# Kernel optimization log

Hardware: AMD Instinct MI355X
Metric: run time of the kernel (lower is better)

## Reference

```python
import jax, jax.numpy as jnp
import numpy as np

V, E, H, A, L = 32000, 512, 1024, 1024, 2
B, T, S = 16, 64, 64


def gru_cell(x, h, W_ih, W_hh, b_ih, b_hh):
    # torch GRUCell math: gates ordered (r, z, n)
    gx = x @ W_ih.T + b_ih
    gh = h @ W_hh.T + b_hh
    xr, xz, xn = jnp.split(gx, 3, axis=-1)
    hr, hz, hn = jnp.split(gh, 3, axis=-1)
    r = jax.nn.sigmoid(xr + hr)
    z = jax.nn.sigmoid(xz + hz)
    n = jnp.tanh(xn + r * hn)
    return (1.0 - z) * n + z * h


def setup_inputs() -> dict:
    key = jax.random.key(0)
    ks = jax.random.split(key, 20)
    s = 0.02
    return {
        "tgt": jax.random.randint(ks[0], (B, T), 0, V),
        "hidden": jax.random.normal(ks[1], (L, B, H), jnp.float32) * 0.1,
        "encoder_outputs": jax.random.normal(ks[2], (B, S, H), jnp.float32),
        "emb": jax.random.normal(ks[3], (V, E), jnp.float32) * s,
        "Wq": jax.random.normal(ks[4], (H, A), jnp.float32) * s,
        "Wk": jax.random.normal(ks[5], (H, A), jnp.float32) * s,
        "v_att": jax.random.normal(ks[6], (A,), jnp.float32) * s,
        "W_ih0": jax.random.normal(ks[7], (3 * H, E + H), jnp.float32) * s,
        "W_hh0": jax.random.normal(ks[8], (3 * H, H), jnp.float32) * s,
        "b_ih0": jnp.zeros((3 * H,), jnp.float32),
        "b_hh0": jnp.zeros((3 * H,), jnp.float32),
        "W_ih1": jax.random.normal(ks[9], (3 * H, H), jnp.float32) * s,
        "W_hh1": jax.random.normal(ks[10], (3 * H, H), jnp.float32) * s,
        "b_ih1": jnp.zeros((3 * H,), jnp.float32),
        "b_hh1": jnp.zeros((3 * H,), jnp.float32),
        "W_out": jax.random.normal(ks[11], (V, H), jnp.float32) * s,
        "b_out": jnp.zeros((V,), jnp.float32),
    }


def reference(tgt, hidden, encoder_outputs, emb, Wq, Wk, v_att,
              W_ih0, W_hh0, b_ih0, b_hh0, W_ih1, W_hh1, b_ih1, b_hh1,
              W_out, b_out):
    # Teacher forcing (ratio=1.0), dropout in eval mode (identity).
    keys_proj = jnp.einsum('bsh,ha->bsa', encoder_outputs, Wk)  # precompute W_k K
    emb_tok = emb[tgt]  # [B,T,E]

    def step(carry, x_t):
        h0, h1 = carry  # each [B,H]
        # Bahdanau attention: query = last-layer hidden
        q = jnp.einsum('bh,ha->ba', h1, Wq)
        scores = jnp.einsum('bsa,a->bs', jnp.tanh(q[:, None, :] + keys_proj), v_att)
        attn = jax.nn.softmax(scores, axis=-1)
        ctx = jnp.einsum('bs,bsh->bh', attn, encoder_outputs)
        rnn_in = jnp.concatenate([x_t, ctx], axis=-1)  # [B, E+H]
        h0n = gru_cell(rnn_in, h0, W_ih0, W_hh0, b_ih0, b_hh0)
        h1n = gru_cell(h0n, h1, W_ih1, W_hh1, b_ih1, b_hh1)
        logits = h1n @ W_out.T + b_out  # [B,V]
        return (h0n, h1n), logits

    (_, _), logits = jax.lax.scan(step, (hidden[0], hidden[1]),
                                  jnp.swapaxes(emb_tok, 0, 1))  # xs: [T,B,E]
    return jnp.swapaxes(logits, 0, 1)  # [B,T,V]
```

## Files before the change

kernel.cpp:

```cpp
#include <hip/hip_runtime.h>
#include <hip/hip_bf16.h>
#include <math.h>

typedef __bf16 bf16x8 __attribute__((ext_vector_type(8)));
typedef float  f32x4  __attribute__((ext_vector_type(4)));

#define MFMA16 __builtin_amdgcn_mfma_f32_16x16x32_bf16

__device__ __forceinline__ float sigm(float x){ return 1.0f/(1.0f+expf(-x)); }
__device__ __forceinline__ f32x4 ld4(const float* p){ return *(const f32x4*)p; }
__device__ __forceinline__ void split2(float x, __bf16* h, __bf16* l){
  __bf16 hh = (__bf16)x; *h = hh; *l = (__bf16)(x - (float)hh);
}

__global__ __launch_bounds__(256) void k_transpose(const float* __restrict__ in,
                                                   float* __restrict__ out, int R, int C){
  __shared__ float tile[32][33];
  int c0 = blockIdx.x*32, r0 = blockIdx.y*32;
  int tx = threadIdx.x & 31, ty = threadIdx.x >> 5;
  for(int i=ty;i<32;i+=8) tile[i][tx] = in[(size_t)(r0+i)*C + c0+tx];
  __syncthreads();
  for(int i=ty;i<32;i+=8) out[(size_t)(c0+i)*R + r0+tx] = tile[tx][i];
}

__global__ __launch_bounds__(256) void k_gather(const int* __restrict__ tgt,
                                                const float* __restrict__ emb,
                                                float* __restrict__ emb_tok){
  int m = blockIdx.x;
  int t = m >> 4, b = m & 15;
  int row = tgt[b*64 + t];
  const float* src = emb + (size_t)row*512;
  float* dst = emb_tok + (size_t)m*512;
  for(int e=threadIdx.x;e<512;e+=256) dst[e] = src[e];
}

__global__ __launch_bounds__(256) void k_gemm_s(
    const float* __restrict__ A, int lda,
    const float* __restrict__ Bt, int ldb,
    const float* __restrict__ bias,
    float* __restrict__ C, int N, int K)
{
  __shared__ __align__(16) __bf16 Ash[128][40];
  __shared__ __align__(16) __bf16 Asl[128][40];
  __shared__ __align__(16) __bf16 Bsh[64][40];
  __shared__ __align__(16) __bf16 Bsl[64][40];
  int tid = threadIdx.x;
  int m0 = blockIdx.x*128, n0 = blockIdx.y*64;
  int lane = tid & 63, wave = tid >> 6;
  int wr = wave >> 1, wc = wave & 1;
  int qq = lane >> 4, rr = lane & 15;
  f32x4 acc[4][2] = {};
  int ar = tid >> 1, ak = (tid & 1)*16;
  int br = tid >> 2, bk = (tid & 3)*8;
  for(int k0=0;k0<K;k0+=32){
    const float* ap = A + (size_t)(m0+ar)*lda + k0 + ak;
    f32x4 a0 = ld4(ap), a1 = ld4(ap+4), a2 = ld4(ap+8), a3 = ld4(ap+12);
    const float* bp = Bt + (size_t)(n0+br)*ldb + k0 + bk;
    f32x4 b0 = ld4(bp), b1 = ld4(bp+4);
    __syncthreads();
    #pragma unroll
    for(int e=0;e<4;++e){
      split2(a0[e], &Ash[ar][ak+e],    &Asl[ar][ak+e]);
      split2(a1[e], &Ash[ar][ak+4+e],  &Asl[ar][ak+4+e]);
      split2(a2[e], &Ash[ar][ak+8+e],  &Asl[ar][ak+8+e]);
      split2(a3[e], &Ash[ar][ak+12+e], &Asl[ar][ak+12+e]);
      split2(b0[e], &Bsh[br][bk+e],    &Bsl[br][bk+e]);
      split2(b1[e], &Bsh[br][bk+4+e],  &Bsl[br][bk+4+e]);
    }
    __syncthreads();
    bf16x8 afh[4], afl[4], bfh[2], bfl[2];
    #pragma unroll
    for(int mi=0;mi<4;++mi){
      afh[mi] = *(const bf16x8*)&Ash[wr*64 + mi*16 + rr][qq*8];
      afl[mi] = *(const bf16x8*)&Asl[wr*64 + mi*16 + rr][qq*8];
    }
    #pragma unroll
    for(int ni=0;ni<2;++ni){
      bfh[ni] = *(const bf16x8*)&Bsh[wc*32 + ni*16 + rr][qq*8];
      bfl[ni] = *(const bf16x8*)&Bsl[wc*32 + ni*16 + rr][qq*8];
    }
    #pragma unroll
    for(int mi=0;mi<4;++mi)
      #pragma unroll
      for(int ni=0;ni<2;++ni){
        acc[mi][ni] = MFMA16(afh[mi], bfh[ni], acc[mi][ni], 0,0,0);
        acc[mi][ni] = MFMA16(afl[mi], bfh[ni], acc[mi][ni], 0,0,0);
        acc[mi][ni] = MFMA16(afh[mi], bfl[ni], acc[mi][ni], 0,0,0);
      }
  }
  #pragma unroll
  for(int mi=0;mi<4;++mi)
    #pragma unroll
    for(int ni=0;ni<2;++ni)
      #pragma unroll
      for(int i=0;i<4;++i){
        int m = m0 + wr*64 + mi*16 + qq*4 + i;
        int n = n0 + wc*32 + ni*16 + rr;
        C[(size_t)m*N + n] = acc[mi][ni][i] + (bias? bias[n] : 0.f);
      }
}

__global__ __launch_bounds__(256) void k_pack_w(const float* __restrict__ W,
                                                __bf16* __restrict__ Wp){
  int jt = blockIdx.x, tid = threadIdx.x;
  #pragma unroll
  for(int it=0; it<8; ++it){
    int pos = it*256 + tid;
    int kt = pos>>6, l = pos&63;
    const float* src = W + (size_t)(jt*16 + (l&15))*1024 + kt*32 + (l>>4)*8;
    f32x4 s0 = ld4(src), s1 = ld4(src+4);
    bf16x8 vh, vl;
    #pragma unroll
    for(int e=0;e<4;++e){
      __bf16 h, lo;
      split2(s0[e], &h, &lo); vh[e]   = h; vl[e]   = lo;
      split2(s1[e], &h, &lo); vh[4+e] = h; vl[4+e] = lo;
    }
    __bf16* dst = Wp + ((size_t)(jt*32 + kt))*1024 + l*8;
    *(bf16x8*)dst       = vh;
    *(bf16x8*)(dst+512) = vl;
  }
}

__global__ __launch_bounds__(256) void k_pack_wT(const float* __restrict__ W, int ldw,
                                                 __bf16* __restrict__ Wp){
  int jt = blockIdx.x, tid = threadIdx.x;
  #pragma unroll
  for(int it=0; it<8; ++it){
    int pos = it*256 + tid;
    int kt = pos>>6, l = pos&63;
    int j = jt*16 + (l&15);
    int kbase = kt*32 + (l>>4)*8;
    bf16x8 vh, vl;
    #pragma unroll
    for(int e=0;e<8;++e){
      float x = W[(size_t)(kbase+e)*ldw + j];
      __bf16 h = (__bf16)x;
      vh[e] = h; vl[e] = (__bf16)(x - (float)h);
    }
    __bf16* dst = Wp + ((size_t)(jt*32 + kt))*1024 + l*8;
    *(bf16x8*)dst       = vh;
    *(bf16x8*)(dst+512) = vl;
  }
}

__global__ __launch_bounds__(256) void k_split_h(const float* __restrict__ hidden,
    __bf16* __restrict__ h0h, __bf16* __restrict__ h0l,
    __bf16* __restrict__ h1h, __bf16* __restrict__ h1l){
  int i = blockIdx.x*256 + threadIdx.x;
  float x = hidden[i];
  if(i < 16384) split2(x, &h0h[i], &h0l[i]);
  else { int j = i - 16384; split2(x, &h1h[j], &h1l[j]); }
}

__global__ __launch_bounds__(256) void k_cvt16(const float* __restrict__ in,
                                               __bf16* __restrict__ out){
  int i = blockIdx.x*256 + threadIdx.x;
  const float* p = in + (size_t)i*8;
  f32x4 f0 = ld4(p), f1 = ld4(p+4);
  bf16x8 v;
  #pragma unroll
  for(int e=0;e<4;++e){ v[e] = (__bf16)f0[e]; v[4+e] = (__bf16)f1[e]; }
  *(bf16x8*)(out + (size_t)i*8) = v;
}

__device__ __forceinline__ void gemv_w8(const __bf16* __restrict__ hh,
                                        const __bf16* __restrict__ hl,
                                        const __bf16* __restrict__ Wp, int jt,
                                        float* __restrict__ out, int ldo,
                                        f32x4* red){
  int tid = threadIdx.x, lane = tid & 63, w = tid >> 6;
  const __bf16* Ah = hh + (lane&15)*1024 + (lane>>4)*8;
  const __bf16* Al = hl + (lane&15)*1024 + (lane>>4)*8;
  const __bf16* Bp = Wp + ((size_t)jt*32 + w*4)*1024 + lane*8;
  f32x4 acc = {0.f,0.f,0.f,0.f};
  #pragma unroll
  for(int kk=0;kk<4;++kk){
    int k0 = (w*4 + kk)*32;
    bf16x8 ah = *(const bf16x8*)(Ah + k0);
    bf16x8 al = *(const bf16x8*)(Al + k0);
    bf16x8 bh = *(const bf16x8*)(Bp + kk*1024);
    bf16x8 bl = *(const bf16x8*)(Bp + kk*1024 + 512);
    acc = MFMA16(ah, bh, acc, 0,0,0);
    acc = MFMA16(al, bh, acc, 0,0,0);
    acc = MFMA16(ah, bl, acc, 0,0,0);
  }
  red[w*64 + lane] = acc;
  __syncthreads();
  if(tid < 64){
    f32x4 s = red[tid];
    #pragma unroll
    for(int k=1;k<8;++k) s += red[k*64 + tid];
    int j = jt*16 + (tid & 15);
    #pragma unroll
    for(int i=0;i<4;++i) out[(size_t)((tid>>4)*4 + i)*ldo + j] = s[i];
  }
}

__global__ __launch_bounds__(512) void k_boot(const __bf16* __restrict__ hh,
                                              const __bf16* __restrict__ hl,
                                              const __bf16* __restrict__ Wp,
                                              float* __restrict__ gh0){
  __shared__ f32x4 red[512];
  gemv_w8(hh, hl, Wp, blockIdx.x, gh0, 3072, red);
}

__global__ __launch_bounds__(512) void k_SA(
    const __bf16* __restrict__ h1h, const __bf16* __restrict__ h1l,
    const __bf16* __restrict__ Whh1p, const __bf16* __restrict__ Wqp,
    const float* __restrict__ kp, const float* __restrict__ v_att,
    float* __restrict__ gh1, float* __restrict__ parts)
{
  __shared__ f32x4 red[512];
  __shared__ float qs[16][16];
  int blk = blockIdx.x, tid = threadIdx.x;
  if(blk < 192){ gemv_w8(h1h, h1l, Whh1p, blk, gh1, 3072, red); return; }
  int slice = blk - 192;
  {
    int lane = tid & 63, w = tid >> 6;
    const __bf16* Ah = h1h + (lane&15)*1024 + (lane>>4)*8;
    const __bf16* Al = h1l + (lane&15)*1024 + (lane>>4)*8;
    const __bf16* Bp = Wqp + ((size_t)slice*32 + w*4)*1024 + lane*8;
    f32x4 acc = {0.f,0.f,0.f,0.f};
    #pragma unroll
    for(int kk=0;kk<4;++kk){
      int k0 = (w*4 + kk)*32;
      bf16x8 ah = *(const bf16x8*)(Ah + k0);
      bf16x8 al = *(const bf16x8*)(Al + k0);
      bf16x8 bh = *(const bf16x8*)(Bp + kk*1024);
      bf16x8 bl = *(const bf16x8*)(Bp + kk*1024 + 512);
      acc = MFMA16(ah, bh, acc, 0,0,0);
      acc = MFMA16(al, bh, acc, 0,0,0);
      acc = MFMA16(ah, bl, acc, 0,0,0);
    }
    red[w*64 + lane] = acc;
    __syncthreads();
    if(tid < 64){
      f32x4 s = red[tid];
      #pragma unroll
      for(int k=1;k<8;++k) s += red[k*64 + tid];
      #pragma unroll
      for(int i=0;i<4;++i) qs[(tid>>4)*4 + i][tid&15] = s[i];
    }
    __syncthreads();
  }
  const float* vp = v_att + slice*16;
  f32x4 v0 = ld4(vp), v1 = ld4(vp+4), v2 = ld4(vp+8), v3 = ld4(vp+12);
  #pragma unroll
  for(int r=0;r<2;++r){
    int pair = r*512 + tid;
    int b = pair >> 6;
    const float* kpr = kp + (size_t)pair*1024 + slice*16;
    f32x4 c0 = ld4(kpr), c1 = ld4(kpr+4), c2 = ld4(kpr+8), c3 = ld4(kpr+12);
    float acc = 0.f;
    #pragma unroll
    for(int e=0;e<4;++e){
      acc += v0[e]*tanhf(qs[b][e]     + c0[e]);
      acc += v1[e]*tanhf(qs[b][4+e]   + c1[e]);
      acc += v2[e]*tanhf(qs[b][8+e]   + c2[e]);
      acc += v3[e]*tanhf(qs[b][12+e]  + c3[e]);
    }
    parts[(size_t)slice*1024 + pair] = acc;
  }
}

__global__ __launch_bounds__(512) void k_SB(int t,
    const float* __restrict__ parts, const float* __restrict__ EW,
    const float* __restrict__ GX0x, const float* __restrict__ gh0,
    const float* __restrict__ b_hh0,
    const float* __restrict__ h0_in, float* __restrict__ h0_out,
    __bf16* __restrict__ h0h, __bf16* __restrict__ h0l)
{
  __shared__ float ssum[256][2];
  __shared__ float sc[4][64];
  __shared__ float sden[4];
  __shared__ float part[8][4][16][3];
  int blk = blockIdx.x, tid = threadIdx.x;
  int jt = blk >> 2, bq = blk & 3;
  {
    int p = tid >> 1, hf = tid & 1;
    int pair = bq*256 + p;
    const float* pp = parts + (size_t)(hf*32)*1024 + pair;
    float s = 0.f;
    #pragma unroll
    for(int k=0;k<32;++k) s += pp[(size_t)k*1024];
    ssum[p][hf] = s;
  }
  __syncthreads();
  if(tid < 256) sc[tid>>6][tid&63] = expf(ssum[tid][0] + ssum[tid][1]);
  __syncthreads();
  if(tid < 4){
    float d = 0.f;
    #pragma unroll
    for(int s2=0;s2<64;++s2) d += sc[tid][s2];
    sden[tid] = d;
  }
  __syncthreads();
  int lane = tid & 63, w = tid >> 6;
  int bl = lane >> 4, jl = lane & 15;
  int b = bq*4 + bl, col = jt*16 + jl;
  float a0=0.f, a1=0.f, a2=0.f;
  const float* ewp = EW + ((size_t)(b*64 + w*8))*3072 + col;
  #pragma unroll
  for(int si=0; si<8; ++si){
    float e = sc[bl][w*8 + si];
    const float* r2 = ewp + (size_t)si*3072;
    a0 += e*r2[0]; a1 += e*r2[1024]; a2 += e*r2[2048];
  }
  part[w][bl][jl][0]=a0; part[w][bl][jl][1]=a1; part[w][bl][jl][2]=a2;
  __syncthreads();
  if(tid < 64){
    int bl2 = tid >> 4, jl2 = tid & 15;
    int b2 = bq*4 + bl2, j = jt*16 + jl2;
    float xr=0.f, xz=0.f, xn=0.f;
    #pragma unroll
    for(int k=0;k<8;++k){ xr+=part[k][bl2][jl2][0]; xz+=part[k][bl2][jl2][1]; xn+=part[k][bl2][jl2][2]; }
    float inv = 1.0f / sden[bl2];
    const float* gx = GX0x + ((size_t)t*16 + b2)*3072 + j;
    const float* g0 = gh0 + (size_t)b2*3072 + j;
    float r = sigm(xr*inv + gx[0]    + g0[0]    + b_hh0[j]);
    float z = sigm(xz*inv + gx[1024] + g0[1024] + b_hh0[1024+j]);
    float n = tanhf(xn*inv + gx[2048] + r*(g0[2048] + b_hh0[2048+j]));
    float hnew = (1.f-z)*n + z*h0_in[b2*1024 + j];
    h0_out[b2*1024 + j] = hnew;
    split2(hnew, &h0h[b2*1024 + j], &h0l[b2*1024 + j]);
  }
}

__global__ __launch_bounds__(512) void k_SC(int t,
    const __bf16* __restrict__ h0h, const __bf16* __restrict__ h0l,
    const __bf16* __restrict__ Wih1p, const __bf16* __restrict__ Whh0p,
    const float* __restrict__ b_ih1, const float* __restrict__ b_hh1,
    const float* __restrict__ gh1,
    const float* __restrict__ h1_in, float* __restrict__ h1_out,
    __bf16* __restrict__ h1h, __bf16* __restrict__ h1l,
    __bf16* __restrict__ Hb, float* __restrict__ gh0)
{
  __shared__ f32x4 red[1536];
  __shared__ float xg[3][16][16];
  int blk = blockIdx.x, tid = threadIdx.x;
  if(blk >= 64){ gemv_w8(h0h, h0l, Whh0p, blk-64, gh0, 3072, red); return; }
  int lane = tid & 63, w = tid >> 6;
  const __bf16* Ah = h0h + (lane&15)*1024 + (lane>>4)*8;
  const __bf16* Al = h0l + (lane&15)*1024 + (lane>>4)*8;
  #pragma unroll
  for(int g=0; g<3; ++g){
    const __bf16* Bp = Wih1p + ((size_t)(g*64 + blk)*32 + w*4)*1024 + lane*8;
    f32x4 acc = {0.f,0.f,0.f,0.f};
    #pragma unroll
    for(int kk=0;kk<4;++kk){
      int k0 = (w*4 + kk)*32;
      bf16x8 ah = *(const bf16x8*)(Ah + k0);
      bf16x8 al = *(const bf16x8*)(Al + k0);
      bf16x8 bh = *(const bf16x8*)(Bp + kk*1024);
      bf16x8 bl = *(const bf16x8*)(Bp + kk*1024 + 512);
      acc = MFMA16(ah, bh, acc, 0,0,0);
      acc = MFMA16(al, bh, acc, 0,0,0);
      acc = MFMA16(ah, bl, acc, 0,0,0);
    }
    red[g*512 + w*64 + lane] = acc;
  }
  __syncthreads();
  if(tid < 192){
    int g = tid >> 6, tt = tid & 63;
    f32x4 s = red[g*512 + tt];
    #pragma unroll
    for(int k=1;k<8;++k) s += red[g*512 + k*64 + tt];
    #pragma unroll
    for(int i=0;i<4;++i) xg[g][(tt>>4)*4 + i][tt&15] = s[i];
  }
  __syncthreads();
  if(tid < 256){
    int b = tid >> 4, jl = tid & 15, j = blk*16 + jl;
    float xr = xg[0][b][jl] + b_ih1[j];
    float xz = xg[1][b][jl] + b_ih1[1024+j];
    float xn = xg[2][b][jl] + b_ih1[2048+j];
    const float* g1 = gh1 + (size_t)b*3072 + j;
    float r = sigm(xr + g1[0]    + b_hh1[j]);
    float z = sigm(xz + g1[1024] + b_hh1[1024+j]);
    float n = tanhf(xn + r*(g1[2048] + b_hh1[2048+j]));
    float hnew = (1.f-z)*n + z*h1_in[b*1024 + j];
    h1_out[b*1024 + j] = hnew;
    split2(hnew, &h1h[b*1024 + j], &h1l[b*1024 + j]);
    Hb[((size_t)t*16 + b)*1024 + j] = (__bf16)hnew;
  }
}

__global__ __launch_bounds__(512) void k_logits(
    const __bf16* __restrict__ Hb, const __bf16* __restrict__ Wb,
    const float* __restrict__ b_out, float* __restrict__ out)
{
  int c = blockIdx.x & 7, j = blockIdx.x >> 3;
  int x = j & 3, y = (j >> 2)*8 + c;
  if(y >= 250) return;
  int tm0 = x*256, tn0 = y*128;
  __shared__ __align__(16) __bf16 As[256][40];
  __shared__ __align__(16) __bf16 Bs[128][40];
  int tid = threadIdx.x;
  int lane = tid & 63, wave = tid >> 6;
  int wr = wave >> 1, wc = wave & 1;
  int qq = lane >> 4, rr = lane & 15;
  f32x4 acc[4][4] = {};
  int ar = tid >> 2, ak = (tid & 3) * 8;
  for(int k0=0;k0<1024;k0+=32){
    bf16x8 a0v = *(const bf16x8*)(Hb + (size_t)(tm0+ar)*1024     + k0 + ak);
    bf16x8 a1v = *(const bf16x8*)(Hb + (size_t)(tm0+ar+128)*1024 + k0 + ak);
    bf16x8 bv  = *(const bf16x8*)(Wb + (size_t)(tn0+ar)*1024     + k0 + ak);
    __syncthreads();
    *(bf16x8*)&As[ar][ak]     = a0v;
    *(bf16x8*)&As[ar+128][ak] = a1v;
    *(bf16x8*)&Bs[ar][ak]     = bv;
    __syncthreads();
    bf16x8 af[4], bfr[4];
    #pragma unroll
    for(int mi=0;mi<4;++mi) af[mi]  = *(const bf16x8*)&As[wr*64 + mi*16 + rr][qq*8];
    #pragma unroll
    for(int ni=0;ni<4;++ni) bfr[ni] = *(const bf16x8*)&Bs[wc*64 + ni*16 + rr][qq*8];
    #pragma unroll
    for(int mi=0;mi<4;++mi)
      #pragma unroll
      for(int ni=0;ni<4;++ni)
        acc[mi][ni] = MFMA16(af[mi], bfr[ni], acc[mi][ni], 0,0,0);
  }
  #pragma unroll
  for(int mi=0;mi<4;++mi)
    #pragma unroll
    for(int ni=0;ni<4;++ni)
      #pragma unroll
      for(int i=0;i<4;++i){
        int m = tm0 + wr*64 + mi*16 + qq*4 + i;
        int v = tn0 + wc*64 + ni*16 + rr;
        int bb = m & 15, tt = m >> 4;
        out[((size_t)bb*64 + tt)*32000 + v] = acc[mi][ni][i] + b_out[v];
      }
}

extern "C" void kernel_launch(void* const* d_in, const int* in_sizes, int n_in,
                              void* d_out, int out_size, void* d_ws, size_t ws_size,
                              hipStream_t stream){
  const int*   tgt    = (const int*)d_in[0];
  const float* hidden = (const float*)d_in[1];
  const float* enc    = (const float*)d_in[2];
  const float* emb    = (const float*)d_in[3];
  const float* Wq     = (const float*)d_in[4];
  const float* Wk     = (const float*)d_in[5];
  const float* v_att  = (const float*)d_in[6];
  const float* W_ih0  = (const float*)d_in[7];
  const float* W_hh0  = (const float*)d_in[8];
  const float* b_ih0  = (const float*)d_in[9];
  const float* b_hh0  = (const float*)d_in[10];
  const float* W_ih1  = (const float*)d_in[11];
  const float* W_hh1  = (const float*)d_in[12];
  const float* b_ih1  = (const float*)d_in[13];
  const float* b_hh1  = (const float*)d_in[14];
  const float* W_out  = (const float*)d_in[15];
  const float* b_out  = (const float*)d_in[16];
  float* out = (float*)d_out;

  float* ws = (float*)d_ws;
  size_t off = 0;
  auto alloc = [&](size_t n){ float* p = ws + off; off += n; return p; };
  float*  kp     = alloc((size_t)1024*1024);
  float*  GX0x   = alloc((size_t)1024*3072);
  float*  EW     = alloc((size_t)1024*3072);
  __bf16* Whh0p  = (__bf16*)alloc((size_t)3072*1024);
  __bf16* Whh1p  = (__bf16*)alloc((size_t)3072*1024);
  __bf16* Wih1p  = (__bf16*)alloc((size_t)3072*1024);
  __bf16* Wqp    = (__bf16*)alloc((size_t)1024*1024);
  float*  gh0    = alloc((size_t)16*3072);
  float*  gh1    = alloc((size_t)16*3072);
  float*  parts  = alloc((size_t)64*1024);
  float*  h0A    = alloc((size_t)16*1024);
  float*  h0B    = alloc((size_t)16*1024);
  float*  h1A    = alloc((size_t)16*1024);
  float*  h1B    = alloc((size_t)16*1024);
  __bf16* h0sh   = (__bf16*)alloc((size_t)8192);
  __bf16* h0sl   = (__bf16*)alloc((size_t)8192);
  __bf16* h1sh   = (__bf16*)alloc((size_t)8192);
  __bf16* h1sl   = (__bf16*)alloc((size_t)8192);
  float*  Hb_f   = alloc((size_t)512*1024);
  __bf16* Hb     = (__bf16*)Hb_f;
  float*  emb_tok = Hb_f;
  float*  WT      = EW;
  __bf16* Woutb   = (__bf16*)ws;
  (void)ws_size; (void)in_sizes; (void)n_in; (void)out_size;

  k_gather<<<1024,256,0,stream>>>(tgt, emb, emb_tok);
  k_transpose<<<dim3(32,32),256,0,stream>>>(Wk, WT, 1024, 1024);
  k_gemm_s<<<dim3(8,16),256,0,stream>>>(enc,1024, WT,1024, nullptr, kp, 1024, 1024);
  k_gemm_s<<<dim3(8,48),256,0,stream>>>(emb_tok,512, W_ih0,1536, b_ih0, GX0x, 3072, 512);
  k_gemm_s<<<dim3(8,48),256,0,stream>>>(enc,1024, W_ih0+512,1536, nullptr, EW, 3072, 1024);
  k_pack_wT<<<64,256,0,stream>>>(Wq, 1024, Wqp);
  k_pack_w<<<192,256,0,stream>>>(W_hh0, Whh0p);
  k_pack_w<<<192,256,0,stream>>>(W_hh1, Whh1p);
  k_pack_w<<<192,256,0,stream>>>(W_ih1, Wih1p);
  k_split_h<<<128,256,0,stream>>>(hidden, h0sh, h0sl, h1sh, h1sl);
  k_boot<<<192,512,0,stream>>>(h0sh, h0sl, Whh0p, gh0);

  for(int t=0;t<64;++t){
    const float* h0i = (t==0)? hidden            : ((t&1)? h0A : h0B);
    float*       h0o = (t&1)? h0B : h0A;
    const float* h1i = (t==0)? hidden + 16*1024  : ((t&1)? h1A : h1B);
    float*       h1o = (t&1)? h1B : h1A;
    k_SA<<<256,512,0,stream>>>(h1sh, h1sl, Whh1p, Wqp, kp, v_att, gh1, parts);
    k_SB<<<256,512,0,stream>>>(t, parts, EW, GX0x, gh0, b_hh0, h0i, h0o, h0sh, h0sl);
    k_SC<<<256,512,0,stream>>>(t, h0sh, h0sl, Wih1p, Whh0p, b_ih1, b_hh1, gh1,
                               h1i, h1o, h1sh, h1sl, Hb, gh0);
  }

  k_cvt16<<<16000,256,0,stream>>>(W_out, Woutb);
  k_logits<<<1024,512,0,stream>>>(Hb, Woutb, b_out, out);
}
```

Before: 2.166 ms.

## Stage recurrent GEMV weights via direct global-to-LDS loads and double-buffer logits A tile

```diff
diff --git a/kernel.cpp b/kernel.cpp
--- a/kernel.cpp
+++ b/kernel.cpp
@@ -6,6 +6,8 @@
 typedef float  f32x4  __attribute__((ext_vector_type(4)));
 
 #define MFMA16 __builtin_amdgcn_mfma_f32_16x16x32_bf16
+#define WAIT_VM0()   { asm volatile("s_waitcnt vmcnt(0)" ::: "memory");   __builtin_amdgcn_sched_barrier(0); }
+#define WAIT_LGKM0() { asm volatile("s_waitcnt lgkmcnt(0)" ::: "memory"); __builtin_amdgcn_sched_barrier(0); }
 
 __device__ __forceinline__ float sigm(float x){ return 1.0f/(1.0f+expf(-x)); }
 __device__ __forceinline__ f32x4 ld4(const float* p){ return *(const f32x4*)p; }
@@ -164,33 +166,48 @@
   *(bf16x8*)(out + (size_t)i*8) = v;
 }
 
-__device__ __forceinline__ void gemv_w8(const __bf16* __restrict__ hh,
-                                        const __bf16* __restrict__ hl,
-                                        const __bf16* __restrict__ Wp, int jt,
-                                        float* __restrict__ out, int ldo,
-                                        f32x4* red){
+__device__ __forceinline__ void stage_tile(const __bf16* __restrict__ Wp, int jt,
+                                           char* stage, int w, int lane){
+  const char* gsrc = (const char*)Wp + (size_t)jt*65536 + (size_t)w*8192 + lane*16;
+  char* ldst = stage + w*8192;
+  #pragma unroll
+  for(int i=0;i<8;++i)
+    __builtin_amdgcn_global_load_lds(
+      (const __attribute__((address_space(1))) unsigned int*)(gsrc + i*1024),
+      (__attribute__((address_space(3))) unsigned int*)(ldst + i*1024), 16, 0, 0);
+}
+
+__device__ __forceinline__ void gemv_lds(const __bf16* __restrict__ hh,
+                                         const __bf16* __restrict__ hl,
+                                         const __bf16* __restrict__ Wp, int jt,
+                                         char* stage, float* __restrict__ out, int ldo){
   int tid = threadIdx.x, lane = tid & 63, w = tid >> 6;
   const __bf16* Ah = hh + (lane&15)*1024 + (lane>>4)*8;
   const __bf16* Al = hl + (lane&15)*1024 + (lane>>4)*8;
-  const __bf16* Bp = Wp + ((size_t)jt*32 + w*4)*1024 + lane*8;
+  bf16x8 ah[4], al[4];
+  #pragma unroll
+  for(int kk=0;kk<4;++kk){
+    int k0 = (w*4+kk)*32;
+    ah[kk] = *(const bf16x8*)(Ah + k0);
+    al[kk] = *(const bf16x8*)(Al + k0);
+  }
+  stage_tile(Wp, jt, stage, w, lane);
+  WAIT_VM0();
   f32x4 acc = {0.f,0.f,0.f,0.f};
   #pragma unroll
   for(int kk=0;kk<4;++kk){
-    int k0 = (w*4 + kk)*32;
-    bf16x8 ah = *(const bf16x8*)(Ah + k0);
-    bf16x8 al = *(const bf16x8*)(Al + k0);
-    bf16x8 bh = *(const bf16x8*)(Bp + kk*1024);
-    bf16x8 bl = *(const bf16x8*)(Bp + kk*1024 + 512);
-    acc = MFMA16(ah, bh, acc, 0,0,0);
-    acc = MFMA16(al, bh, acc, 0,0,0);
-    acc = MFMA16(ah, bl, acc, 0,0,0);
-  }
-  red[w*64 + lane] = acc;
+    bf16x8 bh = *(const bf16x8*)(stage + w*8192 + kk*2048 + lane*16);
+    bf16x8 bl = *(const bf16x8*)(stage + w*8192 + kk*2048 + 1024 + lane*16);
+    acc = MFMA16(ah[kk], bh, acc, 0,0,0);
+    acc = MFMA16(al[kk], bh, acc, 0,0,0);
+    acc = MFMA16(ah[kk], bl, acc, 0,0,0);
+  }
+  *(f32x4*)(stage + w*8192 + lane*16) = acc;
   __syncthreads();
   if(tid < 64){
-    f32x4 s = red[tid];
-    #pragma unroll
-    for(int k=1;k<8;++k) s += red[k*64 + tid];
+    f32x4 s = *(const f32x4*)(stage + tid*16);
+    #pragma unroll
+    for(int k=1;k<8;++k) s += *(const f32x4*)(stage + k*8192 + tid*16);
     int j = jt*16 + (tid & 15);
     #pragma unroll
     for(int i=0;i<4;++i) out[(size_t)((tid>>4)*4 + i)*ldo + j] = s[i];
@@ -201,8 +218,8 @@
                                               const __bf16* __restrict__ hl,
                                               const __bf16* __restrict__ Wp,
                                               float* __restrict__ gh0){
-  __shared__ f32x4 red[512];
-  gemv_w8(hh, hl, Wp, blockIdx.x, gh0, 3072, red);
+  __shared__ __align__(16) char stage[65536];
+  gemv_lds(hh, hl, Wp, blockIdx.x, stage, gh0, 3072);
 }
 
 __global__ __launch_bounds__(512) void k_SA(
@@ -211,39 +228,45 @@
     const float* __restrict__ kp, const float* __restrict__ v_att,
     float* __restrict__ gh1, float* __restrict__ parts)
 {
-  __shared__ f32x4 red[512];
-  __shared__ float qs[16][16];
+  __shared__ __align__(16) char stage[65536];
   int blk = blockIdx.x, tid = threadIdx.x;
-  if(blk < 192){ gemv_w8(h1h, h1l, Whh1p, blk, gh1, 3072, red); return; }
+  if(blk < 192){ gemv_lds(h1h, h1l, Whh1p, blk, stage, gh1, 3072); return; }
   int slice = blk - 192;
+  int lane = tid & 63, w = tid >> 6;
   {
-    int lane = tid & 63, w = tid >> 6;
     const __bf16* Ah = h1h + (lane&15)*1024 + (lane>>4)*8;
     const __bf16* Al = h1l + (lane&15)*1024 + (lane>>4)*8;
-    const __bf16* Bp = Wqp + ((size_t)slice*32 + w*4)*1024 + lane*8;
+    bf16x8 ah[4], al[4];
+    #pragma unroll
+    for(int kk=0;kk<4;++kk){
+      int k0 = (w*4+kk)*32;
+      ah[kk] = *(const bf16x8*)(Ah + k0);
+      al[kk] = *(const bf16x8*)(Al + k0);
+    }
+    stage_tile(Wqp, slice, stage, w, lane);
+    WAIT_VM0();
     f32x4 acc = {0.f,0.f,0.f,0.f};
     #pragma unroll
     for(int kk=0;kk<4;++kk){
-      int k0 = (w*4 + kk)*32;
-      bf16x8 ah = *(const bf16x8*)(Ah + k0);
-      bf16x8 al = *(const bf16x8*)(Al + k0);
-      bf16x8 bh = *(const bf16x8*)(Bp + kk*1024);
-      bf16x8 bl = *(const bf16x8*)(Bp + kk*1024 + 512);
-      acc = MFMA16(ah, bh, acc, 0,0,0);
-      acc = MFMA16(al, bh, acc, 0,0,0);
-      acc = MFMA16(ah, bl, acc, 0,0,0);
-    }
-    red[w*64 + lane] = acc;
+      bf16x8 bh = *(const bf16x8*)(stage + w*8192 + kk*2048 + lane*16);
+      bf16x8 bl = *(const bf16x8*)(stage + w*8192 + kk*2048 + 1024 + lane*16);
+      acc = MFMA16(ah[kk], bh, acc, 0,0,0);
+      acc = MFMA16(al[kk], bh, acc, 0,0,0);
+      acc = MFMA16(ah[kk], bl, acc, 0,0,0);
+    }
+    *(f32x4*)(stage + w*8192 + lane*16) = acc;
     __syncthreads();
     if(tid < 64){
-      f32x4 s = red[tid];
+      f32x4 s = *(const f32x4*)(stage + tid*16);
       #pragma unroll
-      for(int k=1;k<8;++k) s += red[k*64 + tid];
+      for(int k=1;k<8;++k) s += *(const f32x4*)(stage + k*8192 + tid*16);
+      float* qsp = (float*)(stage + 1024);
       #pragma unroll
-      for(int i=0;i<4;++i) qs[(tid>>4)*4 + i][tid&15] = s[i];
+      for(int i=0;i<4;++i) qsp[((tid>>4)*4 + i)*16 + (tid&15)] = s[i];
     }
     __syncthreads();
   }
+  const float* qsp = (const float*)(stage + 1024);
   const float* vp = v_att + slice*16;
   f32x4 v0 = ld4(vp), v1 = ld4(vp+4), v2 = ld4(vp+8), v3 = ld4(vp+12);
   #pragma unroll
@@ -252,13 +275,14 @@
     int b = pair >> 6;
     const float* kpr = kp + (size_t)pair*1024 + slice*16;
     f32x4 c0 = ld4(kpr), c1 = ld4(kpr+4), c2 = ld4(kpr+8), c3 = ld4(kpr+12);
+    const float* qb = qsp + b*16;
     float acc = 0.f;
     #pragma unroll
     for(int e=0;e<4;++e){
-      acc += v0[e]*tanhf(qs[b][e]     + c0[e]);
-      acc += v1[e]*tanhf(qs[b][4+e]   + c1[e]);
-      acc += v2[e]*tanhf(qs[b][8+e]   + c2[e]);
-      acc += v3[e]*tanhf(qs[b][12+e]  + c3[e]);
+      acc += v0[e]*tanhf(qb[e]     + c0[e]);
+      acc += v1[e]*tanhf(qb[4+e]   + c1[e]);
+      acc += v2[e]*tanhf(qb[8+e]   + c2[e]);
+      acc += v3[e]*tanhf(qb[12+e]  + c3[e]);
     }
     parts[(size_t)slice*1024 + pair] = acc;
   }
@@ -278,7 +302,7 @@
   int blk = blockIdx.x, tid = threadIdx.x;
   int jt = blk >> 2, bq = blk & 3;
   {
-    int p = tid >> 1, hf = tid & 1;
+    int hf = tid >> 8, p = tid & 255;
     int pair = bq*256 + p;
     const float* pp = parts + (size_t)(hf*32)*1024 + pair;
     float s = 0.f;
@@ -336,45 +360,62 @@
     __bf16* __restrict__ h1h, __bf16* __restrict__ h1l,
     __bf16* __restrict__ Hb, float* __restrict__ gh0)
 {
-  __shared__ f32x4 red[1536];
-  __shared__ float xg[3][16][16];
+  __shared__ __align__(16) char stage[65536];
   int blk = blockIdx.x, tid = threadIdx.x;
-  if(blk >= 64){ gemv_w8(h0h, h0l, Whh0p, blk-64, gh0, 3072, red); return; }
+  if(blk >= 64){ gemv_lds(h0h, h0l, Whh0p, blk-64, stage, gh0, 3072); return; }
   int lane = tid & 63, w = tid >> 6;
   const __bf16* Ah = h0h + (lane&15)*1024 + (lane>>4)*8;
   const __bf16* Al = h0l + (lane&15)*1024 + (lane>>4)*8;
+  bf16x8 ah[4], al[4];
+  #pragma unroll
+  for(int kk=0;kk<4;++kk){
+    int k0 = (w*4+kk)*32;
+    ah[kk] = *(const bf16x8*)(Ah + k0);
+    al[kk] = *(const bf16x8*)(Al + k0);
+  }
+  f32x4 accg[3];
+  bf16x8 bh[4], bl[4];
+  stage_tile(Wih1p, 0*64 + blk, stage, w, lane);
   #pragma unroll
   for(int g=0; g<3; ++g){
-    const __bf16* Bp = Wih1p + ((size_t)(g*64 + blk)*32 + w*4)*1024 + lane*8;
+    WAIT_VM0();
+    #pragma unroll
+    for(int kk=0;kk<4;++kk){
+      bh[kk] = *(const bf16x8*)(stage + w*8192 + kk*2048 + lane*16);
+      bl[kk] = *(const bf16x8*)(stage + w*8192 + kk*2048 + 1024 + lane*16);
+    }
+    if(g < 2){
+      WAIT_LGKM0();
+      stage_tile(Wih1p, (g+1)*64 + blk, stage, w, lane);
+    }
     f32x4 acc = {0.f,0.f,0.f,0.f};
     #pragma unroll
     for(int kk=0;kk<4;++kk){
-      int k0 = (w*4 + kk)*32;
-      bf16x8 ah = *(const bf16x8*)(Ah + k0);
-      bf16x8 al = *(const bf16x8*)(Al + k0);
-      bf16x8 bh = *(const bf16x8*)(Bp + kk*1024);
-      bf16x8 bl = *(const bf16x8*)(Bp + kk*1024 + 512);
-      acc = MFMA16(ah, bh, acc, 0,0,0);
-      acc = MFMA16(al, bh, acc, 0,0,0);
-      acc = MFMA16(ah, bl, acc, 0,0,0);
-    }
-    red[g*512 + w*64 + lane] = acc;
-  }
-  __syncthreads();
+      acc = MFMA16(ah[kk], bh[kk], acc, 0,0,0);
+      acc = MFMA16(al[kk], bh[kk], acc, 0,0,0);
+      acc = MFMA16(ah[kk], bl[kk], acc, 0,0,0);
+    }
+    accg[g] = acc;
+  }
+  #pragma unroll
+  for(int g=0; g<3; ++g)
+    *(f32x4*)(stage + w*8192 + g*1024 + lane*16) = accg[g];
+  __syncthreads();
+  float* xgp = (float*)(stage + 4096);
   if(tid < 192){
     int g = tid >> 6, tt = tid & 63;
-    f32x4 s = red[g*512 + tt];
-    #pragma unroll
-    for(int k=1;k<8;++k) s += red[g*512 + k*64 + tt];
-    #pragma unroll
-    for(int i=0;i<4;++i) xg[g][(tt>>4)*4 + i][tt&15] = s[i];
+    f32x4 s = *(const f32x4*)(stage + g*1024 + tt*16);
+    #pragma unroll
+    for(int k=1;k<8;++k) s += *(const f32x4*)(stage + k*8192 + g*1024 + tt*16);
+    #pragma unroll
+    for(int i=0;i<4;++i) xgp[g*256 + ((tt>>4)*4 + i)*16 + (tt&15)] = s[i];
   }
   __syncthreads();
   if(tid < 256){
     int b = tid >> 4, jl = tid & 15, j = blk*16 + jl;
-    float xr = xg[0][b][jl] + b_ih1[j];
-    float xz = xg[1][b][jl] + b_ih1[1024+j];
-    float xn = xg[2][b][jl] + b_ih1[2048+j];
+    float xr = xgp[0*256 + b*16 + jl] + b_ih1[j];
+    float xz = xgp[1*256 + b*16 + jl] + b_ih1[1024+j];
+    float xn = xgp[2*256 + b*16 + jl] + b_ih1[2048+j];
     const float* g1 = gh1 + (size_t)b*3072 + j;
     float r = sigm(xr + g1[0]    + b_hh1[j]);
     float z = sigm(xz + g1[1024] + b_hh1[1024+j]);
@@ -394,33 +435,43 @@
   int x = j & 3, y = (j >> 2)*8 + c;
   if(y >= 250) return;
   int tm0 = x*256, tn0 = y*128;
-  __shared__ __align__(16) __bf16 As[256][40];
-  __shared__ __align__(16) __bf16 Bs[128][40];
+  __shared__ __align__(16) __bf16 As[2][256][40];
   int tid = threadIdx.x;
   int lane = tid & 63, wave = tid >> 6;
   int wr = wave >> 1, wc = wave & 1;
   int qq = lane >> 4, rr = lane & 15;
   f32x4 acc[4][4] = {};
   int ar = tid >> 2, ak = (tid & 3) * 8;
+  const __bf16* A0 = Hb + (size_t)(tm0+ar)*1024 + ak;
+  const __bf16* A1 = Hb + (size_t)(tm0+128+ar)*1024 + ak;
+  bf16x8 sa0 = *(const bf16x8*)A0;
+  bf16x8 sa1 = *(const bf16x8*)A1;
+  *(bf16x8*)&As[0][ar][ak]     = sa0;
+  *(bf16x8*)&As[0][128+ar][ak] = sa1;
+  __syncthreads();
   for(int k0=0;k0<1024;k0+=32){
-    bf16x8 a0v = *(const bf16x8*)(Hb + (size_t)(tm0+ar)*1024     + k0 + ak);
-    bf16x8 a1v = *(const bf16x8*)(Hb + (size_t)(tm0+ar+128)*1024 + k0 + ak);
-    bf16x8 bv  = *(const bf16x8*)(Wb + (size_t)(tn0+ar)*1024     + k0 + ak);
-    __syncthreads();
-    *(bf16x8*)&As[ar][ak]     = a0v;
-    *(bf16x8*)&As[ar+128][ak] = a1v;
-    *(bf16x8*)&Bs[ar][ak]     = bv;
-    __syncthreads();
+    int cur = (k0>>5)&1;
+    bool more = (k0+32) < 1024;
+    if(more){
+      sa0 = *(const bf16x8*)(A0 + k0+32);
+      sa1 = *(const bf16x8*)(A1 + k0+32);
+    }
     bf16x8 af[4], bfr[4];
     #pragma unroll
-    for(int mi=0;mi<4;++mi) af[mi]  = *(const bf16x8*)&As[wr*64 + mi*16 + rr][qq*8];
-    #pragma unroll
-    for(int ni=0;ni<4;++ni) bfr[ni] = *(const bf16x8*)&Bs[wc*64 + ni*16 + rr][qq*8];
+    for(int mi=0;mi<4;++mi) af[mi] = *(const bf16x8*)&As[cur][wr*64 + mi*16 + rr][qq*8];
+    #pragma unroll
+    for(int ni=0;ni<4;++ni)
+      bfr[ni] = *(const bf16x8*)(Wb + (size_t)(tn0 + wc*64 + ni*16 + rr)*1024 + k0 + qq*8);
     #pragma unroll
     for(int mi=0;mi<4;++mi)
       #pragma unroll
       for(int ni=0;ni<4;++ni)
         acc[mi][ni] = MFMA16(af[mi], bfr[ni], acc[mi][ni], 0,0,0);
+    if(more){
+      *(bf16x8*)&As[cur^1][ar][ak]     = sa0;
+      *(bf16x8*)&As[cur^1][128+ar][ak] = sa1;
+    }
+    __syncthreads();
   }
   #pragma unroll
   for(int mi=0;mi<4;++mi)
```

New measurement: 2.171 ms. About the same (+0.2%).
